# Optimization experiments

Hardware: AMD Instinct MI355X
Metric: run time of the kernel (lower is better)

The kernel has to match this reference:

```python
import jax, jax.numpy as jnp
import numpy as np

K_NEIGHBORS = 16
NUM_PATCHES = 32
W_NORMAL = 1.0
W_SURFVAR = 1.0


def _knn_centered(points, k):
    """points: [B, N, 3] -> k nearest neighbors re-centered at each point, [B, N, k, 3].
    Distances are computed on stop_gradient(points) to match torch's .detach()."""
    pd = jax.lax.stop_gradient(points)
    # squared pairwise distances [B, N, N] (sqrt is monotone -> topk order identical)
    d2 = jnp.sum((pd[:, :, None, :] - pd[:, None, :, :]) ** 2, axis=-1)
    _, idx = jax.lax.top_k(-d2, k)  # smallest-k indices, [B, N, k]
    knn = jax.vmap(lambda pts, id_: pts[id_])(points, idx)  # [B, N, k, 3]
    return knn - points[:, :, None, :]


def _eig_props(knn):
    """knn: [B, N, k, 3] -> (normal [B,N,3] = eigvec of smallest eigval, eigvals [B,N,3] ascending)."""
    cov = jnp.einsum('bnki,bnkj->bnij', knn, knn)  # [B, N, 3, 3]
    w, v = jnp.linalg.eigh(cov)  # ascending eigenvalues, matches torch.symeig
    return v[..., :, 0], w


def setup_inputs() -> dict:
    key = jax.random.key(0)
    pointCloud = jax.random.normal(key, (4, 8192, 3), dtype=jnp.float32)
    return {"pointCloud": pointCloud}


def reference(pointCloud):
    B, N, _ = pointCloud.shape
    pp = N // NUM_PATCHES

    # global kNN / normals / surface variance
    knn_g = _knn_centered(pointCloud, K_NEIGHBORS)
    nrm_g, w_g = _eig_props(knn_g)

    # patchwise: each patch is an independent small point cloud -> fold patches into batch
    patch_pts = pointCloud.reshape(B * NUM_PATCHES, pp, 3)
    knn_p = _knn_centered(patch_pts, K_NEIGHBORS)
    nrm_p, w_p = _eig_props(knn_p)
    nrm_p = nrm_p.reshape(B, N, 3)

    # normal loss (abs variant, sign-ambiguity-free)
    loss_n = jnp.mean(jnp.linalg.norm(jnp.abs(nrm_p) - jnp.abs(nrm_g), axis=2)) * W_NORMAL

    # surface variance loss: lambda_min / sum(lambda)
    sv_g = w_g[..., 0] / jnp.sum(w_g, axis=-1)            # [B, N]
    sv_p = (w_p[..., 0] / jnp.sum(w_p, axis=-1)).reshape(B, N)
    loss_sv = jnp.mean((sv_p - sv_g) ** 2) * W_SURFVAR

    return jnp.stack([loss_n, loss_sv])  # [2] (original returns list of two [1] tensors)
```

## Files before the change

### kernel.cpp

```cpp
#include <hip/hip_runtime.h>
#include <math.h>

#define KNN 16
#define NPTS 8192
#define PTCH 256
#define NPATCH 32
#define NBATCH 4
#define SSTRIDE 130
#define LAMBDA_T 48.0f

#define GTAB 512
#define RMAX 6.5f
#define GH (RMAX / (float)GTAB)

#define NC 16
#define NCELLS (NC * NC * NC)
#define GMIN -4.2f
#define ICS 1.9047619f

__device__ __forceinline__ float lam_f(float r, float s)
{
    const float C     = 0.063493636f;
    const float SQ2PI = 2.5066283f;
    const float IS2   = 0.70710678f;
    float a = fabsf(r - s), b = r + s;
    float amr = a - r;
    float coefA = amr * amr + 2.f - s * s;
    float I = 2.f * __expf(-0.5f * b * b) - coefA * __expf(-0.5f * a * a)
            + r * SQ2PI * (erff(b * IS2) - erff(a * IS2));
    float M = C * (3.14159265f / r) * I;
    if (s > r) {
        float u = s - r;
        M += 12.566371f * C * (1.2533141f * erff(u * IS2) - u * __expf(-0.5f * u * u));
    }
    return (float)NPTS * M;
}

__device__ __forceinline__ void jrot(double& app, double& aqq, double& apq,
                                     double& arp, double& arq,
                                     double& vp0, double& vq0,
                                     double& vp1, double& vq1,
                                     double& vp2, double& vq2)
{
    double g = apq;
    if (g == 0.0) return;
    double theta = (aqq - app) / (2.0 * g);
    double at = fabs(theta);
    double t = (at > 1.0e154) ? (0.5 / theta)
                              : (copysign(1.0, theta) / (at + sqrt(theta * theta + 1.0)));
    double c = 1.0 / sqrt(t * t + 1.0);
    double s = t * c;
    double tau = s / (1.0 + c);
    app -= t * g;
    aqq += t * g;
    apq = 0.0;
    double rp = arp, rq = arq;
    arp = rp - s * (rq + tau * rp);
    arq = rq + s * (rp - tau * rq);
    double p0 = vp0, q0 = vq0;
    vp0 = p0 - s * (q0 + tau * p0); vq0 = q0 + s * (p0 - tau * q0);
    double p1 = vp1, q1 = vq1;
    vp1 = p1 - s * (q1 + tau * p1); vq1 = q1 + s * (p1 - tau * q1);
    double p2 = vp2, q2 = vq2;
    vp2 = p2 - s * (q2 + tau * p2); vq2 = q2 + s * (p2 - tau * q2);
}

__device__ __forceinline__ void eig3(double a00, double a11, double a22,
                                     double a01, double a02, double a12,
                                     double& nx, double& ny, double& nz,
                                     double& lmin, double& lsum)
{
    double v00 = 1, v01 = 0, v02 = 0;
    double v10 = 0, v11 = 1, v12 = 0;
    double v20 = 0, v21 = 0, v22 = 1;
    double scale = fabs(a00) + fabs(a11) + fabs(a22) + fabs(a01) + fabs(a02) + fabs(a12);
    if (scale > 0.0) {
        for (int sweep = 0; sweep < 6; ++sweep) {
            double off = fabs(a01) + fabs(a02) + fabs(a12);
            if (off <= scale * 1e-15) break;
            jrot(a00, a11, a01, a02, a12, v00, v01, v10, v11, v20, v21);
            jrot(a00, a22, a02, a01, a12, v00, v02, v10, v12, v20, v22);
            jrot(a11, a22, a12, a01, a02, v01, v02, v11, v12, v21, v22);
        }
    }
    lsum = a00 + a11 + a22;
    lmin = a00; nx = v00; ny = v10; nz = v20;
    if (a11 < lmin) { lmin = a11; nx = v01; ny = v11; nz = v21; }
    if (a22 < lmin) { lmin = a22; nx = v02; ny = v12; nz = v22; }
}

__device__ __forceinline__ unsigned mkkey(float d2, unsigned idx) {
    return (__float_as_uint(d2) & 0xFFFFE000u) | idx;
}

__device__ __forceinline__ void insert16(unsigned key, unsigned* L)
{
    L[KNN - 1] = key;
    #pragma unroll
    for (int m = KNN - 1; m >= 1; --m) {
        unsigned a = L[m - 1], b = L[m];
        L[m - 1] = min(a, b);
        L[m]     = max(a, b);
    }
}

__device__ __forceinline__ void merge4(unsigned* L, int lane)
{
    #pragma unroll
    for (int step = 1; step <= 2; step <<= 1) {
        unsigned tmp[KNN];
        #pragma unroll
        for (int m = 0; m < KNN; ++m) tmp[m] = __shfl(L[m], lane ^ step, 64);
        for (int m = 0; m < KNN; ++m) {
            if (tmp[m] >= L[KNN - 1]) break;
            insert16(tmp[m], L);
        }
    }
}

__device__ __forceinline__ unsigned mbcnt64(unsigned long long m) {
    return __builtin_amdgcn_mbcnt_hi((unsigned)(m >> 32),
           __builtin_amdgcn_mbcnt_lo((unsigned)m, 0u));
}

__device__ __forceinline__ int cidx(float v) {
    int i = (int)floorf((v - GMIN) * ICS);
    return min(max(i, 0), NC - 1);
}
__device__ __forceinline__ int cellOf(float x, float y, float z) {
    return (cidx(z) * NC + cidx(y)) * NC + cidx(x);
}

#define BT 1024
__global__ void __launch_bounds__(1024)
build_kernel(const float* __restrict__ pts,
             unsigned* __restrict__ cellStart, float4* __restrict__ sorted,
             float* __restrict__ gtab)
{
    __shared__ unsigned hist[NCELLS];
    __shared__ unsigned part[BT];
    const int b = blockIdx.x;
    const int t = threadIdx.x;
    for (int i = t; i < NCELLS; i += BT) hist[i] = 0u;
    __syncthreads();
    const float* base = pts + (size_t)b * (NPTS * 3);
    float px[8], py[8], pz[8];
    int pc[8];
    #pragma unroll
    for (int k = 0; k < 8; ++k) {
        int i = k * BT + t;
        px[k] = base[i * 3 + 0];
        py[k] = base[i * 3 + 1];
        pz[k] = base[i * 3 + 2];
        pc[k] = cellOf(px[k], py[k], pz[k]);
        atomicAdd(&hist[pc[k]], 1u);
    }
    __syncthreads();
    unsigned loc[4], s = 0;
    #pragma unroll
    for (int i = 0; i < 4; ++i) { loc[i] = s; s += hist[t * 4 + i]; }
    part[t] = s;
    __syncthreads();
    for (int o = 1; o < BT; o <<= 1) {
        unsigned u = (t >= o) ? part[t - o] : 0u;
        __syncthreads();
        part[t] += u;
        __syncthreads();
    }
    unsigned basex = part[t] - s;
    unsigned* csb = cellStart + b * (NCELLS + 1);
    #pragma unroll
    for (int i = 0; i < 4; ++i) {
        unsigned e = basex + loc[i];
        csb[t * 4 + i] = e;
        hist[t * 4 + i] = e;
    }
    if (t == BT - 1) csb[NCELLS] = basex + s;
    __syncthreads();
    float4* sb = sorted + (size_t)b * NPTS;
    #pragma unroll
    for (int k = 0; k < 8; ++k) {
        int i = k * BT + t;
        unsigned slot = atomicAdd(&hist[pc[k]], 1u);
        float4 v;
        v.x = px[k]; v.y = py[k]; v.z = pz[k]; v.w = __uint_as_float((unsigned)i);
        sb[slot] = v;
    }
    if (b == 0 && t < GTAB) {
        float r = fmaxf((float)(t + 1) * GH, 0.01f);
        float lo = 0.f, hi = 12.f;
        #pragma unroll 1
        for (int it = 0; it < 16; ++it) {
            float mid = 0.5f * (lo + hi);
            if (lam_f(r, mid) < LAMBDA_T) lo = mid; else hi = mid;
        }
        gtab[t] = hi;
    }
}

__global__ void __launch_bounds__(256)
fselect_kernel(const float* __restrict__ pts,
               const unsigned* __restrict__ cellStart,
               const float4* __restrict__ sortedp,
               const float* __restrict__ gtab,
               unsigned* __restrict__ idx16)
{
    __shared__ unsigned survl[4 * SSTRIDE];
    const int t = threadIdx.x;
    const int wv = t >> 6;
    const int lane = t & 63;
    const int wq = __builtin_amdgcn_readfirstlane(blockIdx.x * 4 + wv);
    const int b   = wq >> 13;
    const int pos = wq & (NPTS - 1);
    const float* base = pts + (size_t)b * (NPTS * 3);
    const unsigned* cs = cellStart + b * (NCELLS + 1);
    const float4* sp = sortedp + (size_t)b * NPTS;
    unsigned* sl = survl + wv * SSTRIDE;

    const float4 qc = sp[pos];
    const float qx = qc.x, qy = qc.y, qz = qc.z;
    const int oq = b * NPTS + (int)__float_as_uint(qc.w);

    const float r = sqrtf(qx * qx + qy * qy + qz * qz);
    const int gi = min(GTAB - 1, (int)(r * (1.0f / GH)));
    const float g = gtab[gi];
    const float g2 = g * g;

    int ixlo = cidx(qx - g), ixhi = cidx(qx + g);
    int iylo = cidx(qy - g), iyhi = cidx(qy + g);
    int izlo = cidx(qz - g), izhi = cidx(qz + g);
    int nx = ixhi - ixlo + 1;
    int ny = iyhi - iylo + 1;
    int nyz = ny * (izhi - izlo + 1);
    const int lR  = (nyz >= 8) ? 3 : (nyz >= 4) ? 2 : (nyz >= 2) ? 1 : 0;
    const int R   = 1 << lR;
    const int lsl = 6 - lR;
    const unsigned SL = 64u >> lR;
    const unsigned slot = (unsigned)lane & (SL - 1u);
    unsigned cnt = 0;
    #pragma unroll 1
    for (int r0 = 0; r0 < nyz; r0 += 64) {
        int rr = r0 + lane;
        unsigned pk = 0;
        if (rr < nyz) {
            int iz = izlo + rr / ny;
            int iy = iylo + (rr - (rr / ny) * ny);
            int cb = (iz * NC + iy) * NC + ixlo;
            unsigned sB = cs[cb];
            pk = sB | ((cs[cb + nx] - sB) << 14);
        }
        int rmax = min(nyz - r0, 64);
        int gcount = (rmax + R - 1) >> lR;
        #pragma unroll 1
        for (int gg = 0; gg < gcount; ++gg) {
            unsigned pkm = __shfl(pk, (gg << lR) + (lane >> lsl), 64);
            unsigned sBm = pkm & 0x3FFFu;
            unsigned lm  = pkm >> 14;
            #pragma unroll 1
            for (unsigned st = slot; ; st += 2u * SL) {
                bool in0 = st < lm;
                if (!__any(in0 ? 1 : 0)) break;
                unsigned st1 = st + SL;
                bool in1 = st1 < lm;
                float4 c0 = sp[min(sBm + st,  (unsigned)(NPTS - 1))];
                float4 c1 = sp[min(sBm + st1, (unsigned)(NPTS - 1))];
                float dx0 = qx - c0.x, dy0 = qy - c0.y, dz0 = qz - c0.z;
                float d20 = dx0 * dx0 + dy0 * dy0 + dz0 * dz0;
                float dx1 = qx - c1.x, dy1 = qy - c1.y, dz1 = qz - c1.z;
                float d21 = dx1 * dx1 + dy1 * dy1 + dz1 * dz1;
                bool p0 = in0 && (d20 < g2);
                bool p1 = in1 && (d21 < g2);
                unsigned long long m0 = __ballot(p0);
                unsigned long long m1 = __ballot(p1);
                if (p0) {
                    unsigned sw = min(cnt + mbcnt64(m0), (unsigned)(SSTRIDE - 1));
                    sl[sw] = mkkey(d20, __float_as_uint(c0.w));
                }
                unsigned cn = cnt + (unsigned)__popcll(m0);
                if (p1) {
                    unsigned sw = min(cn + mbcnt64(m1), (unsigned)(SSTRIDE - 1));
                    sl[sw] = mkkey(d21, __float_as_uint(c1.w));
                }
                cnt = cn + (unsigned)__popcll(m1);
            }
        }
    }

    bool valid = (cnt >= KNN) && (cnt <= 128u);
    if (valid) {
        unsigned k0 = (lane < (int)cnt)      ? sl[lane]      : 0xFFFFFFFFu;
        unsigned k1 = (lane + 64 < (int)cnt) ? sl[lane + 64] : 0xFFFFFFFFu;
        unsigned r0 = 0, r1 = 0;
        #pragma unroll 4
        for (unsigned m = 0; m < cnt; ++m) {
            unsigned km = sl[m];
            r0 += (km < k0) ? 1u : 0u;
            r1 += (km < k1) ? 1u : 0u;
        }
        unsigned cand = 0;
        if (lane < (int)cnt && r0 == 15u) cand = k0;
        if (lane + 64 < (int)cnt && r1 == 15u) cand = k1;
        #pragma unroll
        for (int o = 1; o < 64; o <<= 1)
            cand = max(cand, (unsigned)__shfl_xor((int)cand, o, 64));
        float upper = __uint_as_float((cand & 0xFFFFE000u) + 0x2000u);
        valid = (upper < g2 * 0.999f - 1e-5f);
        if (valid) {
            if (lane < (int)cnt && r0 < 16u)
                idx16[(size_t)oq * 32 + r0] = k0 & 0x1FFFu;
            if (lane + 64 < (int)cnt && r1 < 16u)
                idx16[(size_t)oq * 32 + r1] = k1 & 0x1FFFu;
        }
    }
    if (!valid && lane == 0) {
        unsigned gl[KNN];
        #pragma unroll
        for (int m = 0; m < KNN; ++m) gl[m] = 0xFFFFFFFFu;
        #pragma unroll 1
        for (int i = 0; i < NPTS; ++i) {
            float cx = base[i * 3 + 0];
            float cy = base[i * 3 + 1];
            float cz = base[i * 3 + 2];
            float dx = qx - cx, dy = qy - cy, dz = qz - cz;
            float d2 = dx * dx + dy * dy + dz * dz;
            unsigned k = mkkey(d2, (unsigned)i);
            if (k < gl[KNN - 1]) insert16(k, gl);
        }
        unsigned* dst = idx16 + (size_t)oq * 32;
        #pragma unroll
        for (int m = 0; m < KNN; ++m) dst[m] = gl[m] & 0x1FFFu;
    }
}

__global__ void __launch_bounds__(256)
pselect_kernel(const float* __restrict__ pts, unsigned* __restrict__ idx16)
{
    __shared__ float4 pbuf4[PTCH];
    const int t = threadIdx.x;
    const int w = t >> 6;
    const int lane = t & 63;
    const int p = blockIdx.x;
    const int quarter = blockIdx.y;
    const int b = blockIdx.z;
    const float* base = pts + (size_t)b * (NPTS * 3);

    {
        const float* src = base + p * (PTCH * 3);
        float* dst = (float*)pbuf4;
        #pragma unroll
        for (int s = 0; s < 3; ++s) {
            int f = t + s * 256;
            int j = f / 3;
            int c = f - 3 * j;
            dst[j * 4 + c] = src[f];
        }
    }
    __syncthreads();

    const int qq = lane >> 2;
    const int h = lane & 3;
    const int qlocal = quarter * 64 + w * 16 + qq;
    float4 qv = pbuf4[qlocal];
    const float pqx = qv.x, pqy = qv.y, pqz = qv.z;

    unsigned pl[KNN];
    #pragma unroll
    for (int m = 0; m < KNN; ++m) pl[m] = 0xFFFFFFFFu;
    const int j0 = h * 64;
    #pragma unroll 4
    for (int j = j0; j < j0 + 64; ++j) {
        float4 c = pbuf4[j];
        float dx = pqx - c.x, dy = pqy - c.y, dz = pqz - c.z;
        float d2 = dx * dx + dy * dy + dz * dz;
        unsigned k = mkkey(d2, (unsigned)j);
        if (k < pl[KNN - 1]) insert16(k, pl);
    }
    merge4(pl, lane);
    if (h == 0) {
        int qid = b * NPTS + p * PTCH + qlocal;
        unsigned* dst = idx16 + (size_t)qid * 32 + 16;
        #pragma unroll
        for (int m = 0; m < KNN; ++m)
            dst[m] = (unsigned)(p * PTCH) + (pl[m] & 0x1FFFu);
    }
}

__global__ void __launch_bounds__(256)
eig_loss_kernel(const float* __restrict__ pts,
                const unsigned* __restrict__ idx16,
                double* __restrict__ partials)
{
    __shared__ double sln[4], slv[4];
    const int t = threadIdx.x;
    const int e = blockIdx.x * 256 + t;
    const int qid = e >> 1;
    const int b = qid >> 13;
    const int qi = qid & (NPTS - 1);
    const float* base = pts + (size_t)b * (NPTS * 3);

    const double qxd = (double)base[qi * 3 + 0];
    const double qyd = (double)base[qi * 3 + 1];
    const double qzd = (double)base[qi * 3 + 2];

    const unsigned* L = idx16 + (size_t)qid * 32 + (e & 1) * 16;
    double c00 = 0, c11 = 0, c22 = 0, c01 = 0, c02 = 0, c12 = 0;
    #pragma unroll
    for (int m = 0; m < KNN; ++m) {
        int idx = (int)L[m];
        double dx = (double)base[idx * 3 + 0] - qxd;
        double dy = (double)base[idx * 3 + 1] - qyd;
        double dz = (double)base[idx * 3 + 2] - qzd;
        c00 += dx * dx; c11 += dy * dy; c22 += dz * dz;
        c01 += dx * dy; c02 += dx * dz; c12 += dy * dz;
    }
    double nx, ny, nz, lmin, lsum;
    eig3(c00, c11, c22, c01, c02, c12, nx, ny, nz, lmin, lsum);
    double sv = lmin / lsum;

    double onx = __shfl_xor(nx, 1, 64);
    double ony = __shfl_xor(ny, 1, 64);
    double onz = __shfl_xor(nz, 1, 64);
    double osv = __shfl_xor(sv, 1, 64);

    double ln = 0.0, lsv = 0.0;
    if ((e & 1) == 0) {
        double dx = fabs(onx) - fabs(nx);
        double dy = fabs(ony) - fabs(ny);
        double dz = fabs(onz) - fabs(nz);
        ln  = sqrt(dx * dx + dy * dy + dz * dz);
        double ds = osv - sv;
        lsv = ds * ds;
    }
    #pragma unroll
    for (int o = 32; o > 0; o >>= 1) {
        ln  += __shfl_down(ln, o);
        lsv += __shfl_down(lsv, o);
    }
    const int w = t >> 6;
    if ((t & 63) == 0) { sln[w] = ln; slv[w] = lsv; }
    __syncthreads();
    if (t == 0) {
        partials[blockIdx.x * 2 + 0] = sln[0] + sln[1] + sln[2] + sln[3];
        partials[blockIdx.x * 2 + 1] = slv[0] + slv[1] + slv[2] + slv[3];
    }
}

__global__ void __launch_bounds__(256)
reduce_kernel(const double* __restrict__ partials, float* __restrict__ out)
{
    __shared__ double sln[4], slv[4];
    const int t = threadIdx.x;
    double a = partials[t * 2 + 0];
    double c = partials[t * 2 + 1];
    #pragma unroll
    for (int o = 32; o > 0; o >>= 1) {
        a += __shfl_down(a, o);
        c += __shfl_down(c, o);
    }
    if ((t & 63) == 0) { sln[t >> 6] = a; slv[t >> 6] = c; }
    __syncthreads();
    if (t == 0) {
        const double inv = 1.0 / (double)(NBATCH * NPTS);
        out[0] = (float)((sln[0] + sln[1] + sln[2] + sln[3]) * inv);
        out[1] = (float)((slv[0] + slv[1] + slv[2] + slv[3]) * inv);
    }
}

extern "C" void kernel_launch(void* const* d_in, const int* in_sizes, int n_in,
                              void* d_out, int out_size, void* d_ws, size_t ws_size,
                              hipStream_t stream)
{
    const float* pts = (const float*)d_in[0];
    float* out = (float*)d_out;

    unsigned char* ws = (unsigned char*)d_ws;
    unsigned* cellStart = (unsigned*)(ws);
    float4*   sorted    = (float4*)  (ws + 65552);
    float*    gtab      = (float*)   (ws + 589840);
    unsigned* idx16     = (unsigned*)(ws + 591888);
    double*   partials  = (double*)  (ws + 4786192);

    hipLaunchKernelGGL(build_kernel, dim3(NBATCH), dim3(BT), 0, stream,
                       pts, cellStart, sorted, gtab);
    hipLaunchKernelGGL(fselect_kernel, dim3(NBATCH * NPTS / 4), dim3(256), 0, stream,
                       pts, cellStart, sorted, gtab, idx16);
    hipLaunchKernelGGL(pselect_kernel, dim3(NPATCH, 4, NBATCH), dim3(256), 0, stream,
                       pts, idx16);
    hipLaunchKernelGGL(eig_loss_kernel, dim3(NBATCH * NPTS * 2 / 256), dim3(256),
                       0, stream, pts, idx16, partials);
    hipLaunchKernelGGL(reduce_kernel, dim3(1), dim3(256), 0, stream,
                       partials, out);
}
```

Measured before the change: 136.3 us.

## Merge global and patch selection kernels, fold final reduction into eig kernel

The global kNN selection and the patchwise selection now run as two block ranges of one combined launch, so the patch blocks can fill the GPU alongside the global ones instead of waiting for a separate launch. The final reduction kernel is removed: the last eig_loss block, found through an atomic counter reset in build_kernel, reduces the partials and writes the output. This cuts the pipeline from five launches to three. It costs a larger shared-memory footprint per block for the combined kernel and relies on a threadfence plus atomic last-block pattern.

Measured after the change: 143.6 us. 5.4% more time.

```diff
diff --git a/kernel.cpp b/kernel.cpp
--- a/kernel.cpp
+++ b/kernel.cpp
@@ -17,6 +17,9 @@
 #define NCELLS (NC * NC * NC)
 #define GMIN -4.2f
 #define ICS 1.9047619f
+
+#define FBLK (NBATCH * NPTS / 4)
+#define PBLK (NPATCH * 4 * NBATCH)
 
 __device__ __forceinline__ float lam_f(float r, float s)
 {
@@ -135,12 +138,13 @@
 __global__ void __launch_bounds__(1024)
 build_kernel(const float* __restrict__ pts,
              unsigned* __restrict__ cellStart, float4* __restrict__ sorted,
-             float* __restrict__ gtab)
+             float* __restrict__ gtab, unsigned* __restrict__ done)
 {
     __shared__ unsigned hist[NCELLS];
     __shared__ unsigned part[BT];
     const int b = blockIdx.x;
     const int t = threadIdx.x;
+    if (b == 0 && t == 0) done[0] = 0u;
     for (int i = t; i < NCELLS; i += BT) hist[i] = 0u;
     __syncthreads();
     const float* base = pts + (size_t)b * (NPTS * 3);
@@ -199,198 +203,199 @@
 }
 
 __global__ void __launch_bounds__(256)
-fselect_kernel(const float* __restrict__ pts,
-               const unsigned* __restrict__ cellStart,
-               const float4* __restrict__ sortedp,
-               const float* __restrict__ gtab,
-               unsigned* __restrict__ idx16)
+sel_kernel(const float* __restrict__ pts,
+           const unsigned* __restrict__ cellStart,
+           const float4* __restrict__ sortedp,
+           const float* __restrict__ gtab,
+           unsigned* __restrict__ idx16)
 {
     __shared__ unsigned survl[4 * SSTRIDE];
-    const int t = threadIdx.x;
-    const int wv = t >> 6;
-    const int lane = t & 63;
-    const int wq = __builtin_amdgcn_readfirstlane(blockIdx.x * 4 + wv);
-    const int b   = wq >> 13;
-    const int pos = wq & (NPTS - 1);
-    const float* base = pts + (size_t)b * (NPTS * 3);
-    const unsigned* cs = cellStart + b * (NCELLS + 1);
-    const float4* sp = sortedp + (size_t)b * NPTS;
-    unsigned* sl = survl + wv * SSTRIDE;
-
-    const float4 qc = sp[pos];
-    const float qx = qc.x, qy = qc.y, qz = qc.z;
-    const int oq = b * NPTS + (int)__float_as_uint(qc.w);
-
-    const float r = sqrtf(qx * qx + qy * qy + qz * qz);
-    const int gi = min(GTAB - 1, (int)(r * (1.0f / GH)));
-    const float g = gtab[gi];
-    const float g2 = g * g;
-
-    int ixlo = cidx(qx - g), ixhi = cidx(qx + g);
-    int iylo = cidx(qy - g), iyhi = cidx(qy + g);
-    int izlo = cidx(qz - g), izhi = cidx(qz + g);
-    int nx = ixhi - ixlo + 1;
-    int ny = iyhi - iylo + 1;
-    int nyz = ny * (izhi - izlo + 1);
-    const int lR  = (nyz >= 8) ? 3 : (nyz >= 4) ? 2 : (nyz >= 2) ? 1 : 0;
-    const int R   = 1 << lR;
-    const int lsl = 6 - lR;
-    const unsigned SL = 64u >> lR;
-    const unsigned slot = (unsigned)lane & (SL - 1u);
-    unsigned cnt = 0;
-    #pragma unroll 1
-    for (int r0 = 0; r0 < nyz; r0 += 64) {
-        int rr = r0 + lane;
-        unsigned pk = 0;
-        if (rr < nyz) {
-            int iz = izlo + rr / ny;
-            int iy = iylo + (rr - (rr / ny) * ny);
-            int cb = (iz * NC + iy) * NC + ixlo;
-            unsigned sB = cs[cb];
-            pk = sB | ((cs[cb + nx] - sB) << 14);
-        }
-        int rmax = min(nyz - r0, 64);
-        int gcount = (rmax + R - 1) >> lR;
-        #pragma unroll 1
-        for (int gg = 0; gg < gcount; ++gg) {
-            unsigned pkm = __shfl(pk, (gg << lR) + (lane >> lsl), 64);
-            unsigned sBm = pkm & 0x3FFFu;
-            unsigned lm  = pkm >> 14;
-            #pragma unroll 1
-            for (unsigned st = slot; ; st += 2u * SL) {
-                bool in0 = st < lm;
-                if (!__any(in0 ? 1 : 0)) break;
-                unsigned st1 = st + SL;
-                bool in1 = st1 < lm;
-                float4 c0 = sp[min(sBm + st,  (unsigned)(NPTS - 1))];
-                float4 c1 = sp[min(sBm + st1, (unsigned)(NPTS - 1))];
-                float dx0 = qx - c0.x, dy0 = qy - c0.y, dz0 = qz - c0.z;
-                float d20 = dx0 * dx0 + dy0 * dy0 + dz0 * dz0;
-                float dx1 = qx - c1.x, dy1 = qy - c1.y, dz1 = qz - c1.z;
-                float d21 = dx1 * dx1 + dy1 * dy1 + dz1 * dz1;
-                bool p0 = in0 && (d20 < g2);
-                bool p1 = in1 && (d21 < g2);
-                unsigned long long m0 = __ballot(p0);
-                unsigned long long m1 = __ballot(p1);
-                if (p0) {
-                    unsigned sw = min(cnt + mbcnt64(m0), (unsigned)(SSTRIDE - 1));
-                    sl[sw] = mkkey(d20, __float_as_uint(c0.w));
-                }
-                unsigned cn = cnt + (unsigned)__popcll(m0);
-                if (p1) {
-                    unsigned sw = min(cn + mbcnt64(m1), (unsigned)(SSTRIDE - 1));
-                    sl[sw] = mkkey(d21, __float_as_uint(c1.w));
-                }
-                cnt = cn + (unsigned)__popcll(m1);
-            }
-        }
-    }
-
-    bool valid = (cnt >= KNN) && (cnt <= 128u);
-    if (valid) {
-        unsigned k0 = (lane < (int)cnt)      ? sl[lane]      : 0xFFFFFFFFu;
-        unsigned k1 = (lane + 64 < (int)cnt) ? sl[lane + 64] : 0xFFFFFFFFu;
-        unsigned r0 = 0, r1 = 0;
-        #pragma unroll 4
-        for (unsigned m = 0; m < cnt; ++m) {
-            unsigned km = sl[m];
-            r0 += (km < k0) ? 1u : 0u;
-            r1 += (km < k1) ? 1u : 0u;
-        }
-        unsigned cand = 0;
-        if (lane < (int)cnt && r0 == 15u) cand = k0;
-        if (lane + 64 < (int)cnt && r1 == 15u) cand = k1;
-        #pragma unroll
-        for (int o = 1; o < 64; o <<= 1)
-            cand = max(cand, (unsigned)__shfl_xor((int)cand, o, 64));
-        float upper = __uint_as_float((cand & 0xFFFFE000u) + 0x2000u);
-        valid = (upper < g2 * 0.999f - 1e-5f);
-        if (valid) {
-            if (lane < (int)cnt && r0 < 16u)
-                idx16[(size_t)oq * 32 + r0] = k0 & 0x1FFFu;
-            if (lane + 64 < (int)cnt && r1 < 16u)
-                idx16[(size_t)oq * 32 + r1] = k1 & 0x1FFFu;
-        }
-    }
-    if (!valid && lane == 0) {
-        unsigned gl[KNN];
-        #pragma unroll
-        for (int m = 0; m < KNN; ++m) gl[m] = 0xFFFFFFFFu;
-        #pragma unroll 1
-        for (int i = 0; i < NPTS; ++i) {
-            float cx = base[i * 3 + 0];
-            float cy = base[i * 3 + 1];
-            float cz = base[i * 3 + 2];
-            float dx = qx - cx, dy = qy - cy, dz = qz - cz;
-            float d2 = dx * dx + dy * dy + dz * dz;
-            unsigned k = mkkey(d2, (unsigned)i);
-            if (k < gl[KNN - 1]) insert16(k, gl);
-        }
-        unsigned* dst = idx16 + (size_t)oq * 32;
-        #pragma unroll
-        for (int m = 0; m < KNN; ++m) dst[m] = gl[m] & 0x1FFFu;
-    }
-}
-
-__global__ void __launch_bounds__(256)
-pselect_kernel(const float* __restrict__ pts, unsigned* __restrict__ idx16)
-{
     __shared__ float4 pbuf4[PTCH];
     const int t = threadIdx.x;
-    const int w = t >> 6;
     const int lane = t & 63;
-    const int p = blockIdx.x;
-    const int quarter = blockIdx.y;
-    const int b = blockIdx.z;
-    const float* base = pts + (size_t)b * (NPTS * 3);
-
-    {
-        const float* src = base + p * (PTCH * 3);
-        float* dst = (float*)pbuf4;
+
+    if (blockIdx.x < FBLK) {
+        const int wv = t >> 6;
+        const int wq = __builtin_amdgcn_readfirstlane(blockIdx.x * 4 + wv);
+        const int b   = wq >> 13;
+        const int pos = wq & (NPTS - 1);
+        const float* base = pts + (size_t)b * (NPTS * 3);
+        const unsigned* cs = cellStart + b * (NCELLS + 1);
+        const float4* sp = sortedp + (size_t)b * NPTS;
+        unsigned* sl = survl + wv * SSTRIDE;
+
+        const float4 qc = sp[pos];
+        const float qx = qc.x, qy = qc.y, qz = qc.z;
+        const int oq = b * NPTS + (int)__float_as_uint(qc.w);
+
+        const float r = sqrtf(qx * qx + qy * qy + qz * qz);
+        const int gi = min(GTAB - 1, (int)(r * (1.0f / GH)));
+        const float g = gtab[gi];
+        const float g2 = g * g;
+
+        int ixlo = cidx(qx - g), ixhi = cidx(qx + g);
+        int iylo = cidx(qy - g), iyhi = cidx(qy + g);
+        int izlo = cidx(qz - g), izhi = cidx(qz + g);
+        int nx = ixhi - ixlo + 1;
+        int ny = iyhi - iylo + 1;
+        int nyz = ny * (izhi - izlo + 1);
+        const int lR  = (nyz >= 8) ? 3 : (nyz >= 4) ? 2 : (nyz >= 2) ? 1 : 0;
+        const int R   = 1 << lR;
+        const int lsl = 6 - lR;
+        const unsigned SL = 64u >> lR;
+        const unsigned slot = (unsigned)lane & (SL - 1u);
+        unsigned cnt = 0;
+        #pragma unroll 1
+        for (int r0 = 0; r0 < nyz; r0 += 64) {
+            int rr = r0 + lane;
+            unsigned pk = 0;
+            if (rr < nyz) {
+                int iz = izlo + rr / ny;
+                int iy = iylo + (rr - (rr / ny) * ny);
+                int cb = (iz * NC + iy) * NC + ixlo;
+                unsigned sB = cs[cb];
+                pk = sB | ((cs[cb + nx] - sB) << 14);
+            }
+            int rmax = min(nyz - r0, 64);
+            int gcount = (rmax + R - 1) >> lR;
+            #pragma unroll 1
+            for (int gg = 0; gg < gcount; ++gg) {
+                unsigned pkm = __shfl(pk, (gg << lR) + (lane >> lsl), 64);
+                unsigned sBm = pkm & 0x3FFFu;
+                unsigned lm  = pkm >> 14;
+                #pragma unroll 1
+                for (unsigned st = slot; ; st += 2u * SL) {
+                    bool in0 = st < lm;
+                    if (!__any(in0 ? 1 : 0)) break;
+                    unsigned st1 = st + SL;
+                    bool in1 = st1 < lm;
+                    float4 c0 = sp[min(sBm + st,  (unsigned)(NPTS - 1))];
+                    float4 c1 = sp[min(sBm + st1, (unsigned)(NPTS - 1))];
+                    float dx0 = qx - c0.x, dy0 = qy - c0.y, dz0 = qz - c0.z;
+                    float d20 = dx0 * dx0 + dy0 * dy0 + dz0 * dz0;
+                    float dx1 = qx - c1.x, dy1 = qy - c1.y, dz1 = qz - c1.z;
+                    float d21 = dx1 * dx1 + dy1 * dy1 + dz1 * dz1;
+                    bool p0 = in0 && (d20 < g2);
+                    bool p1 = in1 && (d21 < g2);
+                    unsigned long long m0 = __ballot(p0);
+                    unsigned long long m1 = __ballot(p1);
+                    if (p0) {
+                        unsigned sw = min(cnt + mbcnt64(m0), (unsigned)(SSTRIDE - 1));
+                        sl[sw] = mkkey(d20, __float_as_uint(c0.w));
+                    }
+                    unsigned cn = cnt + (unsigned)__popcll(m0);
+                    if (p1) {
+                        unsigned sw = min(cn + mbcnt64(m1), (unsigned)(SSTRIDE - 1));
+                        sl[sw] = mkkey(d21, __float_as_uint(c1.w));
+                    }
+                    cnt = cn + (unsigned)__popcll(m1);
+                }
+            }
+        }
+
+        bool valid = (cnt >= KNN) && (cnt <= 128u);
+        if (valid) {
+            unsigned k0 = (lane < (int)cnt)      ? sl[lane]      : 0xFFFFFFFFu;
+            unsigned k1 = (lane + 64 < (int)cnt) ? sl[lane + 64] : 0xFFFFFFFFu;
+            unsigned r0 = 0, r1 = 0;
+            #pragma unroll 4
+            for (unsigned m = 0; m < cnt; ++m) {
+                unsigned km = sl[m];
+                r0 += (km < k0) ? 1u : 0u;
+                r1 += (km < k1) ? 1u : 0u;
+            }
+            unsigned cand = 0;
+            if (lane < (int)cnt && r0 == 15u) cand = k0;
+            if (lane + 64 < (int)cnt && r1 == 15u) cand = k1;
+            #pragma unroll
+            for (int o = 1; o < 64; o <<= 1)
+                cand = max(cand, (unsigned)__shfl_xor((int)cand, o, 64));
+            float upper = __uint_as_float((cand & 0xFFFFE000u) + 0x2000u);
+            valid = (upper < g2 * 0.999f - 1e-5f);
+            if (valid) {
+                if (lane < (int)cnt && r0 < 16u)
+                    idx16[(size_t)oq * 32 + r0] = k0 & 0x1FFFu;
+                if (lane + 64 < (int)cnt && r1 < 16u)
+                    idx16[(size_t)oq * 32 + r1] = k1 & 0x1FFFu;
+            }
+        }
+        if (!valid && lane == 0) {
+            unsigned gl[KNN];
+            #pragma unroll
+            for (int m = 0; m < KNN; ++m) gl[m] = 0xFFFFFFFFu;
+            #pragma unroll 1
+            for (int i = 0; i < NPTS; ++i) {
+                float cx = base[i * 3 + 0];
+                float cy = base[i * 3 + 1];
+                float cz = base[i * 3 + 2];
+                float dx = qx - cx, dy = qy - cy, dz = qz - cz;
+                float d2 = dx * dx + dy * dy + dz * dz;
+                unsigned k = mkkey(d2, (unsigned)i);
+                if (k < gl[KNN - 1]) insert16(k, gl);
+            }
+            unsigned* dst = idx16 + (size_t)oq * 32;
+            #pragma unroll
+            for (int m = 0; m < KNN; ++m) dst[m] = gl[m] & 0x1FFFu;
+        }
+    } else {
+        const int pb = blockIdx.x - FBLK;
+        const int w = t >> 6;
+        const int p = pb & (NPATCH - 1);
+        const int quarter = (pb >> 5) & 3;
+        const int b = pb >> 7;
+        const float* base = pts + (size_t)b * (NPTS * 3);
+
+        {
+            const float* src = base + p * (PTCH * 3);
+            float* dst = (float*)pbuf4;
+            #pragma unroll
+            for (int s = 0; s < 3; ++s) {
+                int f = t + s * 256;
+                int j = f / 3;
+                int c = f - 3 * j;
+                dst[j * 4 + c] = src[f];
+            }
+        }
+        __syncthreads();
+
+        const int qq = lane >> 2;
+        const int h = lane & 3;
+        const int qlocal = quarter * 64 + w * 16 + qq;
+        float4 qv = pbuf4[qlocal];
+        const float pqx = qv.x, pqy = qv.y, pqz = qv.z;
+
+        unsigned pl[KNN];
         #pragma unroll
-        for (int s = 0; s < 3; ++s) {
-            int f = t + s * 256;
-            int j = f / 3;
-            int c = f - 3 * j;
-            dst[j * 4 + c] = src[f];
-        }
-    }
-    __syncthreads();
-
-    const int qq = lane >> 2;
-    const int h = lane & 3;
-    const int qlocal = quarter * 64 + w * 16 + qq;
-    float4 qv = pbuf4[qlocal];
-    const float pqx = qv.x, pqy = qv.y, pqz = qv.z;
-
-    unsigned pl[KNN];
-    #pragma unroll
-    for (int m = 0; m < KNN; ++m) pl[m] = 0xFFFFFFFFu;
-    const int j0 = h * 64;
-    #pragma unroll 4
-    for (int j = j0; j < j0 + 64; ++j) {
-        float4 c = pbuf4[j];
-        float dx = pqx - c.x, dy = pqy - c.y, dz = pqz - c.z;
-        float d2 = dx * dx + dy * dy + dz * dz;
-        unsigned k = mkkey(d2, (unsigned)j);
-        if (k < pl[KNN - 1]) insert16(k, pl);
-    }
-    merge4(pl, lane);
-    if (h == 0) {
-        int qid = b * NPTS + p * PTCH + qlocal;
-        unsigned* dst = idx16 + (size_t)qid * 32 + 16;
-        #pragma unroll
-        for (int m = 0; m < KNN; ++m)
-            dst[m] = (unsigned)(p * PTCH) + (pl[m] & 0x1FFFu);
+        for (int m = 0; m < KNN; ++m) pl[m] = 0xFFFFFFFFu;
+        const int j0 = h * 64;
+        #pragma unroll 4
+        for (int j = j0; j < j0 + 64; ++j) {
+            float4 c = pbuf4[j];
+            float dx = pqx - c.x, dy = pqy - c.y, dz = pqz - c.z;
+            float d2 = dx * dx + dy * dy + dz * dz;
+            unsigned k = mkkey(d2, (unsigned)j);
+            if (k < pl[KNN - 1]) insert16(k, pl);
+        }
+        merge4(pl, lane);
+        if (h == 0) {
+            int qid = b * NPTS + p * PTCH + qlocal;
+            unsigned* dst = idx16 + (size_t)qid * 32 + 16;
+            #pragma unroll
+            for (int m = 0; m < KNN; ++m)
+                dst[m] = (unsigned)(p * PTCH) + (pl[m] & 0x1FFFu);
+        }
     }
 }
 
 __global__ void __launch_bounds__(256)
 eig_loss_kernel(const float* __restrict__ pts,
                 const unsigned* __restrict__ idx16,
-                double* __restrict__ partials)
+                double* __restrict__ partials,
+                unsigned* __restrict__ done,
+                float* __restrict__ out)
 {
     __shared__ double sln[4], slv[4];
+    __shared__ unsigned isLast;
     const int t = threadIdx.x;
     const int e = blockIdx.x * 256 + t;
     const int qid = e >> 1;
@@ -442,27 +447,25 @@
     if (t == 0) {
         partials[blockIdx.x * 2 + 0] = sln[0] + sln[1] + sln[2] + sln[3];
         partials[blockIdx.x * 2 + 1] = slv[0] + slv[1] + slv[2] + slv[3];
-    }
-}
-
-__global__ void __launch_bounds__(256)
-reduce_kernel(const double* __restrict__ partials, float* __restrict__ out)
-{
-    __shared__ double sln[4], slv[4];
-    const int t = threadIdx.x;
-    double a = partials[t * 2 + 0];
-    double c = partials[t * 2 + 1];
-    #pragma unroll
-    for (int o = 32; o > 0; o >>= 1) {
-        a += __shfl_down(a, o);
-        c += __shfl_down(c, o);
-    }
-    if ((t & 63) == 0) { sln[t >> 6] = a; slv[t >> 6] = c; }
-    __syncthreads();
-    if (t == 0) {
-        const double inv = 1.0 / (double)(NBATCH * NPTS);
-        out[0] = (float)((sln[0] + sln[1] + sln[2] + sln[3]) * inv);
-        out[1] = (float)((slv[0] + slv[1] + slv[2] + slv[3]) * inv);
+        __threadfence();
+        isLast = (atomicAdd(done, 1u) == (unsigned)(gridDim.x - 1)) ? 1u : 0u;
+    }
+    __syncthreads();
+    if (isLast) {
+        double a = partials[t * 2 + 0];
+        double c = partials[t * 2 + 1];
+        #pragma unroll
+        for (int o = 32; o > 0; o >>= 1) {
+            a += __shfl_down(a, o);
+            c += __shfl_down(c, o);
+        }
+        if ((t & 63) == 0) { sln[t >> 6] = a; slv[t >> 6] = c; }
+        __syncthreads();
+        if (t == 0) {
+            const double inv = 1.0 / (double)(NBATCH * NPTS);
+            out[0] = (float)((sln[0] + sln[1] + sln[2] + sln[3]) * inv);
+            out[1] = (float)((slv[0] + slv[1] + slv[2] + slv[3]) * inv);
+        }
     }
 }
 
@@ -477,17 +480,14 @@
     unsigned* cellStart = (unsigned*)(ws);
     float4*   sorted    = (float4*)  (ws + 65552);
     float*    gtab      = (float*)   (ws + 589840);
-    unsigned* idx16     = (unsigned*)(ws + 591888);
-    double*   partials  = (double*)  (ws + 4786192);
+    unsigned* done      = (unsigned*)(ws + 591888);
+    unsigned* idx16     = (unsigned*)(ws + 591904);
+    double*   partials  = (double*)  (ws + 4786208);
 
     hipLaunchKernelGGL(build_kernel, dim3(NBATCH), dim3(BT), 0, stream,
-                       pts, cellStart, sorted, gtab);
-    hipLaunchKernelGGL(fselect_kernel, dim3(NBATCH * NPTS / 4), dim3(256), 0, stream,
+                       pts, cellStart, sorted, gtab, done);
+    hipLaunchKernelGGL(sel_kernel, dim3(FBLK + PBLK), dim3(256), 0, stream,
                        pts, cellStart, sorted, gtab, idx16);
-    hipLaunchKernelGGL(pselect_kernel, dim3(NPATCH, 4, NBATCH), dim3(256), 0, stream,
-                       pts, idx16);
     hipLaunchKernelGGL(eig_loss_kernel, dim3(NBATCH * NPTS * 2 / 256), dim3(256),
-                       0, stream, pts, idx16, partials);
-    hipLaunchKernelGGL(reduce_kernel, dim3(1), dim3(256), 0, stream,
-                       partials, out);
-}
+                       0, stream, pts, idx16, partials, done, out);
+}
```
